# Performance work log

Measured on AMD Instinct MI355X. Metric: run time of the kernel, lower is better.

## Reference

```python
import jax, jax.numpy as jnp
import numpy as np
from math import atanh

B, T, D_IN, H = 16, 1024, 512, 1024
INIT_A = atanh(0.95)


def setup_inputs() -> dict:
    key = jax.random.key(0)
    k1, k2, k3, k4 = jax.random.split(key, 4)
    x = jax.random.normal(k1, (B, T, D_IN), dtype=jnp.float32)
    h0 = jax.random.normal(k2, (B, H), dtype=jnp.float32)
    # raw_a initialized near atanh(0.95) as in the module, with small jitter
    raw_a = INIT_A + 0.01 * jax.random.normal(k3, (H,), dtype=jnp.float32)
    # xavier-uniform for W_x.weight [H, D_IN]
    limit = float(np.sqrt(6.0 / (D_IN + H)))
    W = jax.random.uniform(k4, (H, D_IN), dtype=jnp.float32, minval=-limit, maxval=limit)
    b = jnp.zeros((H,), dtype=jnp.float32)
    return {"x": x, "h0": h0, "raw_a": raw_a, "W": W, "b": b}


def reference(x, h0, raw_a, W, b):
    # h_t = a * h_{t-1} + W x_t + b, computed via cumprod/cumsum parallel-scan trick
    a = jnp.tanh(raw_a)                                   # [H] (rho is None)
    z = jnp.einsum('btd,hd->bth', x, W) + b               # [B,T,H]
    A = jnp.broadcast_to(a, (x.shape[1], a.shape[0]))     # [T,H]
    p = jnp.cumprod(A, axis=0)[None]                      # [1,T,H], p[t] = a^(t+1)
    v = jnp.cumsum(z / jnp.maximum(p, 1e-12), axis=1)     # [B,T,H]
    h = v * p + p * h0[:, None, :]                        # include initial state
    zero_mask = (jnp.abs(a) < 1e-6)[None, None, :]        # degenerate a ~ 0 channels
    h = jnp.where(zero_mask, z, h)
    return h
```

## Files before the change

kernel.cpp:

```cpp
#include <hip/hip_runtime.h>
#include <cstdint>

#define B_DIM 16
#define T_DIM 1024
#define DK    512
#define H_DIM 1024

#define TCH    128
#define NCH    (T_DIM / TCH)
#define NB     128
#define NSTRIP (H_DIM / NB)
#define NKT    16
#define BKQ    4

typedef __bf16 bf16x8 __attribute__((ext_vector_type(8)));
typedef __bf16 bf16x4 __attribute__((ext_vector_type(4)));
typedef float  f32x4  __attribute__((ext_vector_type(4)));

typedef __attribute__((address_space(1))) unsigned int* as1p;
typedef __attribute__((address_space(3))) unsigned int* as3p;

__device__ __forceinline__ void async_cp16(const void* g, void* l) {
  __builtin_amdgcn_global_load_lds((as1p)(uint64_t)g,
                                   (as3p)(uint32_t)(uint64_t)l, 16, 0, 0);
}

__global__ __launch_bounds__(256) void prep(const float* __restrict__ x,
                                            __bf16* __restrict__ xbt,
                                            const float* __restrict__ W,
                                            __bf16* __restrict__ wbT,
                                            const float* __restrict__ raw_a,
                                            float4* __restrict__ meta,
                                            unsigned long long* __restrict__ flags) {
  const int bid = blockIdx.x, tid = threadIdx.x;
  if (bid < 4096) {
    const int g = bid * 256 + tid;
    const int b = g >> 16;
    const int r = g & 65535;
    const int kq = ((r >> 12) << 2) | (tid & 3);
    const int t  = (((r >> 6) & 63) << 4) | ((tid & 63) >> 2);
    const float* src = x + ((size_t)(b * T_DIM + t) * DK + kq * 8);
    f32x4 v0 = ((const f32x4*)src)[0];
    f32x4 v1 = ((const f32x4*)src)[1];
    bf16x8 o;
    o[0] = (__bf16)v0.x; o[1] = (__bf16)v0.y; o[2] = (__bf16)v0.z; o[3] = (__bf16)v0.w;
    o[4] = (__bf16)v1.x; o[5] = (__bf16)v1.y; o[6] = (__bf16)v1.z; o[7] = (__bf16)v1.w;
    *(bf16x8*)(xbt + ((size_t)(b * 64 + kq) * T_DIM + t) * 8) = o;
  } else if (bid < 4608) {
    const int i = (bid - 4096) * 256 + tid;
    const int h  = i >> 7;
    const int k0 = (i & 127) * 4;
    f32x4 v = ((const f32x4*)W)[i];
    bf16x4 o;
    o.x = (__bf16)v.x; o.y = (__bf16)v.y; o.z = (__bf16)v.z; o.w = (__bf16)v.w;
    *(bf16x4*)(wbT + ((size_t)(k0 >> 3) * H_DIM + h) * 8 + (k0 & 7)) = o;
  } else if (bid < 4612) {
    const int h = (bid - 4608) * 256 + tid;
    const float a = tanhf(raw_a[h]);
    const float la2 = log2f(fabsf(a));
    meta[h] = make_float4(a, la2, (a < 0.f) ? 1.f : 0.f, (fabsf(a) < 1e-6f) ? 1.f : 0.f);
  } else {
    flags[(bid - 4612) * 256 + tid] = 0ULL;
  }
}

__global__ __launch_bounds__(256, 3) void fused_rnn(
    const __bf16* __restrict__ xbt,
    const __bf16* __restrict__ wbT,
    const float* __restrict__ bias,
    const float4* __restrict__ meta,
    const float* __restrict__ h0g,
    unsigned long long* __restrict__ flags,
    float* __restrict__ out) {
  __shared__ __align__(16) __bf16 As[3][BKQ][TCH][8];
  __shared__ __align__(16) __bf16 Bs[3][BKQ][NB][8];
  __shared__ float chunkTot[2][NB];
  __shared__ float colCarry[NB];

  const int tid  = threadIdx.x;
  const int wave = tid >> 6;
  const int lane = tid & 63;
  const int q  = lane >> 4;
  const int c  = lane & 15;
  const int rw = wave & 1;
  const int cg = wave >> 1;

  const int bid   = blockIdx.x;
  const int g     = bid & 127;
  const int strip = bid >> 7;
  const int b     = g >> 3;
  const int chunk = g & 7;
  const int t0    = chunk * TCH;
  const int n0    = strip * NB;

  float bias_j[4], la2_j[4], a_j[4], ai_j[4], sgn_j[4], h0_j[4];
  bool zm_j[4];
#pragma unroll
  for (int j = 0; j < 4; ++j) {
    const int col = n0 + cg * 64 + j * 16 + c;
    bias_j[j] = bias[col];
    const float4 mt = meta[col];
    a_j[j]   = mt.x;
    la2_j[j] = mt.y;
    ai_j[j]  = 1.f / mt.x;
    sgn_j[j] = (mt.z != 0.f) ? -1.f : 1.f;
    zm_j[j]  = mt.w != 0.f;
    h0_j[j]  = h0g[(size_t)b * H_DIM + col];
  }

  auto stage = [&](int kt, int buf) {
    const int kq0 = kt * BKQ;
#pragma unroll
    for (int it = 0; it < 2; ++it) {
      const int s = it * 256 + tid;
      const int kq = s >> 7, row = s & 127;
      async_cp16(xbt + ((size_t)(b * 64 + kq0 + kq) * T_DIM + t0 + row) * 8,
                 &As[buf][kq][row][0]);
    }
#pragma unroll
    for (int it = 0; it < 2; ++it) {
      const int s = it * 256 + tid;
      const int kq = s >> 7, col = s & 127;
      async_cp16(wbT + ((size_t)(kq0 + kq) * H_DIM + n0 + col) * 8,
                 &Bs[buf][kq][col][0]);
    }
  };

  f32x4 acc[4][4];
#pragma unroll
  for (int i = 0; i < 4; ++i)
#pragma unroll
    for (int j = 0; j < 4; ++j)
      acc[i][j] = (f32x4){bias_j[j], bias_j[j], bias_j[j], bias_j[j]};

  stage(0, 0); stage(1, 1); stage(2, 2);

  int buf = 0;
  for (int kt = 0; kt < NKT; ++kt) {
    if (kt < NKT - 2)       asm volatile("s_waitcnt vmcnt(8)" ::: "memory");
    else if (kt == NKT - 2) asm volatile("s_waitcnt vmcnt(4)" ::: "memory");
    else                    asm volatile("s_waitcnt vmcnt(0)" ::: "memory");
    __builtin_amdgcn_s_barrier();
    bf16x8 af[4], bfr[4];
#pragma unroll
    for (int i = 0; i < 4; ++i)
      af[i] = *(const bf16x8*)(&As[buf][q][rw * 64 + i * 16 + c][0]);
#pragma unroll
    for (int j = 0; j < 4; ++j)
      bfr[j] = *(const bf16x8*)(&Bs[buf][q][cg * 64 + j * 16 + c][0]);
#pragma unroll
    for (int i = 0; i < 4; ++i)
#pragma unroll
      for (int j = 0; j < 4; ++j)
        acc[i][j] = __builtin_amdgcn_mfma_f32_16x16x32_bf16(af[i], bfr[j], acc[i][j], 0, 0, 0);
    __builtin_amdgcn_sched_barrier(0);
    __builtin_amdgcn_s_barrier();
    if (kt < NKT - 3) stage(kt + 3, buf);
    buf = (buf == 2) ? 0 : buf + 1;
  }

  float base_[4][4];
  float icarry[4] = {0.f, 0.f, 0.f, 0.f};
#pragma unroll
  for (int i = 0; i < 4; ++i) {
    const int tp10 = t0 + rw * 64 + i * 16 + q * 4 + 1;
#pragma unroll
    for (int j = 0; j < 4; ++j) {
      float u = __builtin_amdgcn_exp2f(-la2_j[j] * (float)tp10) * sgn_j[j];
      f32x4 wv;
#pragma unroll
      for (int r = 0; r < 4; ++r) {
        const float uu = fminf(u, 1e12f);
        const float inv = (u < 0.f) ? 1e12f : uu;
        wv[r] = acc[i][j][r] * inv;
        u *= ai_j[j];
      }
      const float pr0 = wv[0];
      const float pr1 = pr0 + wv[1];
      const float pr2 = pr1 + wv[2];
      const float pr3 = pr2 + wv[3];
      const float x1 = __shfl_xor(pr3, 16, 64);
      const float x2 = __shfl_xor(pr3, 32, 64);
      const float x3 = __shfl_xor(pr3, 48, 64);
      float sq = 0.f;
      if (q >= 2) sq += x2 + x3;
      if (q & 1) sq += x1;
      const float base = icarry[j] + sq;
      base_[i][j] = base;
      acc[i][j] = (f32x4){base + pr0, base + pr1, base + pr2, base + pr3};
      icarry[j] += pr3 + x1 + x2 + x3;
    }
  }
  if (q == 0) {
#pragma unroll
    for (int j = 0; j < 4; ++j) chunkTot[rw][cg * 64 + j * 16 + c] = icarry[j];
  }
  __syncthreads();

  if (tid < NB) {
    const int col = tid;
    const size_t fb = ((size_t)b * NSTRIP + strip) * NCH * NB;
    const float tot = chunkTot[0][col] + chunkTot[1][col];
    atomicExch(&flags[fb + (size_t)chunk * NB + col],
               (1ULL << 32) | (unsigned long long)__float_as_uint(tot));
    float s = 0.f;
    for (int p = 0; p < chunk; ++p) {
      unsigned long long v = atomicAdd(&flags[fb + (size_t)p * NB + col], 0ULL);
      while (!(v >> 32)) {
        __builtin_amdgcn_s_sleep(4);
        v = atomicAdd(&flags[fb + (size_t)p * NB + col], 0ULL);
      }
      s += __uint_as_float((unsigned int)v);
    }
    colCarry[col] = s;
  }
  __syncthreads();

  float cc_[4];
#pragma unroll
  for (int j = 0; j < 4; ++j) {
    const int colL = cg * 64 + j * 16 + c;
    float s = colCarry[colL];
    if (rw) s += chunkTot[0][colL];
    cc_[j] = s + h0_j[j];
  }
#pragma unroll
  for (int i = 0; i < 4; ++i) {
    const int tp10 = t0 + rw * 64 + i * 16 + q * 4 + 1;
#pragma unroll
    for (int j = 0; j < 4; ++j) {
      float pv = __builtin_amdgcn_exp2f(la2_j[j] * (float)tp10) * sgn_j[j];
      const int col = n0 + cg * 64 + j * 16 + c;
#pragma unroll
      for (int r = 0; r < 4; ++r) {
        const int tl = t0 + rw * 64 + i * 16 + q * 4 + r;
        const float hv = pv * (acc[i][j][r] + cc_[j]);
        const float wr = acc[i][j][r] - ((r == 0) ? base_[i][j] : acc[i][j][r - 1]);
        out[(size_t)(b * T_DIM + tl) * H_DIM + col] = zm_j[j] ? wr * 1e-12f : hv;
        pv *= a_j[j];
      }
    }
  }
}

extern "C" void kernel_launch(void* const* d_in, const int* in_sizes, int n_in,
                              void* d_out, int out_size, void* d_ws, size_t ws_size,
                              hipStream_t stream) {
  const float* x     = (const float*)d_in[0];
  const float* h0    = (const float*)d_in[1];
  const float* raw_a = (const float*)d_in[2];
  const float* W     = (const float*)d_in[3];
  const float* bias  = (const float*)d_in[4];
  float* out = (float*)d_out;

  char* ws = (char*)d_ws;
  __bf16* xbt = (__bf16*)(ws);
  __bf16* wbT = (__bf16*)(ws + 16777216);
  float4* meta = (float4*)(ws + 16777216 + 1048576);
  unsigned long long* flags =
      (unsigned long long*)(ws + 16777216 + 1048576 + 16384);

  prep<<<5124, 256, 0, stream>>>(x, xbt, W, wbT, raw_a, meta, flags);
  fused_rnn<<<1024, 256, 0, stream>>>(xbt, wbT, bias, meta, h0, flags, out);
}
```

Measured before the change: 124.3 us.

## Fuse x fp32-to-bf16 conversion into GEMM loads, drop separate x prepass

```diff
diff --git a/kernel.cpp b/kernel.cpp
--- a/kernel.cpp
+++ b/kernel.cpp
@@ -11,7 +11,6 @@
 #define NB     128
 #define NSTRIP (H_DIM / NB)
 #define NKT    16
-#define BKQ    4
 
 typedef __bf16 bf16x8 __attribute__((ext_vector_type(8)));
 typedef __bf16 bf16x4 __attribute__((ext_vector_type(4)));
@@ -25,55 +24,40 @@
                                    (as3p)(uint32_t)(uint64_t)l, 16, 0, 0);
 }
 
-__global__ __launch_bounds__(256) void prep(const float* __restrict__ x,
-                                            __bf16* __restrict__ xbt,
-                                            const float* __restrict__ W,
+__global__ __launch_bounds__(256) void prep(const float* __restrict__ W,
                                             __bf16* __restrict__ wbT,
                                             const float* __restrict__ raw_a,
                                             float4* __restrict__ meta,
                                             unsigned long long* __restrict__ flags) {
   const int bid = blockIdx.x, tid = threadIdx.x;
-  if (bid < 4096) {
-    const int g = bid * 256 + tid;
-    const int b = g >> 16;
-    const int r = g & 65535;
-    const int kq = ((r >> 12) << 2) | (tid & 3);
-    const int t  = (((r >> 6) & 63) << 4) | ((tid & 63) >> 2);
-    const float* src = x + ((size_t)(b * T_DIM + t) * DK + kq * 8);
-    f32x4 v0 = ((const f32x4*)src)[0];
-    f32x4 v1 = ((const f32x4*)src)[1];
-    bf16x8 o;
-    o[0] = (__bf16)v0.x; o[1] = (__bf16)v0.y; o[2] = (__bf16)v0.z; o[3] = (__bf16)v0.w;
-    o[4] = (__bf16)v1.x; o[5] = (__bf16)v1.y; o[6] = (__bf16)v1.z; o[7] = (__bf16)v1.w;
-    *(bf16x8*)(xbt + ((size_t)(b * 64 + kq) * T_DIM + t) * 8) = o;
-  } else if (bid < 4608) {
-    const int i = (bid - 4096) * 256 + tid;
+  if (bid < 512) {
+    const int i = bid * 256 + tid;
     const int h  = i >> 7;
     const int k0 = (i & 127) * 4;
     f32x4 v = ((const f32x4*)W)[i];
     bf16x4 o;
     o.x = (__bf16)v.x; o.y = (__bf16)v.y; o.z = (__bf16)v.z; o.w = (__bf16)v.w;
     *(bf16x4*)(wbT + ((size_t)(k0 >> 3) * H_DIM + h) * 8 + (k0 & 7)) = o;
-  } else if (bid < 4612) {
-    const int h = (bid - 4608) * 256 + tid;
+  } else if (bid < 516) {
+    const int h = (bid - 512) * 256 + tid;
     const float a = tanhf(raw_a[h]);
     const float la2 = log2f(fabsf(a));
     meta[h] = make_float4(a, la2, (a < 0.f) ? 1.f : 0.f, (fabsf(a) < 1e-6f) ? 1.f : 0.f);
   } else {
-    flags[(bid - 4612) * 256 + tid] = 0ULL;
+    flags[(bid - 516) * 256 + tid] = 0ULL;
   }
 }
 
 __global__ __launch_bounds__(256, 3) void fused_rnn(
-    const __bf16* __restrict__ xbt,
+    const float* __restrict__ xf,
     const __bf16* __restrict__ wbT,
     const float* __restrict__ bias,
     const float4* __restrict__ meta,
     const float* __restrict__ h0g,
     unsigned long long* __restrict__ flags,
     float* __restrict__ out) {
-  __shared__ __align__(16) __bf16 As[3][BKQ][TCH][8];
-  __shared__ __align__(16) __bf16 Bs[3][BKQ][NB][8];
+  __shared__ __align__(16) float  Asf[2][8][TCH][4];
+  __shared__ __align__(16) __bf16 Bs[2][4][NB][8];
   __shared__ float chunkTot[2][NB];
   __shared__ float colCarry[NB];
 
@@ -93,12 +77,72 @@
   const int t0    = chunk * TCH;
   const int n0    = strip * NB;
 
-  float bias_j[4], la2_j[4], a_j[4], ai_j[4], sgn_j[4], h0_j[4];
+  float bias_j[4];
+#pragma unroll
+  for (int j = 0; j < 4; ++j) bias_j[j] = bias[n0 + cg * 64 + j * 16 + c];
+
+  const float* const xB = xf + (size_t)(b * T_DIM + t0) * DK;
+
+  auto stage = [&](int kt, int buf) {
+#pragma unroll
+    for (int it = 0; it < 4; ++it) {
+      const int s = it * 256 + tid;
+      const int kq4 = s >> 7, row = s & 127;
+      async_cp16(xB + (size_t)row * DK + kt * 32 + kq4 * 4,
+                 &Asf[buf][kq4][row][0]);
+    }
+#pragma unroll
+    for (int it = 0; it < 2; ++it) {
+      const int s = it * 256 + tid;
+      const int kq = s >> 7, col = s & 127;
+      async_cp16(wbT + ((size_t)(kt * 4 + kq) * H_DIM + n0 + col) * 8,
+                 &Bs[buf][kq][col][0]);
+    }
+  };
+
+  f32x4 acc[4][4];
+#pragma unroll
+  for (int i = 0; i < 4; ++i)
+#pragma unroll
+    for (int j = 0; j < 4; ++j)
+      acc[i][j] = (f32x4){bias_j[j], bias_j[j], bias_j[j], bias_j[j]};
+
+  stage(0, 0); stage(1, 1);
+
+  for (int kt = 0; kt < NKT; ++kt) {
+    const int buf = kt & 1;
+    if (kt < NKT - 1) asm volatile("s_waitcnt vmcnt(6)" ::: "memory");
+    else              asm volatile("s_waitcnt vmcnt(0)" ::: "memory");
+    __builtin_amdgcn_s_barrier();
+    bf16x8 af[4], bfr[4];
+#pragma unroll
+    for (int i = 0; i < 4; ++i) {
+      const int row = rw * 64 + i * 16 + c;
+      const f32x4 a0 = *(const f32x4*)(&Asf[buf][2 * q][row][0]);
+      const f32x4 a1 = *(const f32x4*)(&Asf[buf][2 * q + 1][row][0]);
+      bf16x8 t;
+      t[0] = (__bf16)a0.x; t[1] = (__bf16)a0.y; t[2] = (__bf16)a0.z; t[3] = (__bf16)a0.w;
+      t[4] = (__bf16)a1.x; t[5] = (__bf16)a1.y; t[6] = (__bf16)a1.z; t[7] = (__bf16)a1.w;
+      af[i] = t;
+    }
+#pragma unroll
+    for (int j = 0; j < 4; ++j)
+      bfr[j] = *(const bf16x8*)(&Bs[buf][q][cg * 64 + j * 16 + c][0]);
+#pragma unroll
+    for (int i = 0; i < 4; ++i)
+#pragma unroll
+      for (int j = 0; j < 4; ++j)
+        acc[i][j] = __builtin_amdgcn_mfma_f32_16x16x32_bf16(af[i], bfr[j], acc[i][j], 0, 0, 0);
+    __builtin_amdgcn_sched_barrier(0);
+    __builtin_amdgcn_s_barrier();
+    if (kt < NKT - 2) stage(kt + 2, buf);
+  }
+
+  float la2_j[4], a_j[4], ai_j[4], sgn_j[4], h0_j[4];
   bool zm_j[4];
 #pragma unroll
   for (int j = 0; j < 4; ++j) {
     const int col = n0 + cg * 64 + j * 16 + c;
-    bias_j[j] = bias[col];
     const float4 mt = meta[col];
     a_j[j]   = mt.x;
     la2_j[j] = mt.y;
@@ -106,57 +150,6 @@
     sgn_j[j] = (mt.z != 0.f) ? -1.f : 1.f;
     zm_j[j]  = mt.w != 0.f;
     h0_j[j]  = h0g[(size_t)b * H_DIM + col];
-  }
-
-  auto stage = [&](int kt, int buf) {
-    const int kq0 = kt * BKQ;
-#pragma unroll
-    for (int it = 0; it < 2; ++it) {
-      const int s = it * 256 + tid;
-      const int kq = s >> 7, row = s & 127;
-      async_cp16(xbt + ((size_t)(b * 64 + kq0 + kq) * T_DIM + t0 + row) * 8,
-                 &As[buf][kq][row][0]);
-    }
-#pragma unroll
-    for (int it = 0; it < 2; ++it) {
-      const int s = it * 256 + tid;
-      const int kq = s >> 7, col = s & 127;
-      async_cp16(wbT + ((size_t)(kq0 + kq) * H_DIM + n0 + col) * 8,
-                 &Bs[buf][kq][col][0]);
-    }
-  };
-
-  f32x4 acc[4][4];
-#pragma unroll
-  for (int i = 0; i < 4; ++i)
-#pragma unroll
-    for (int j = 0; j < 4; ++j)
-      acc[i][j] = (f32x4){bias_j[j], bias_j[j], bias_j[j], bias_j[j]};
-
-  stage(0, 0); stage(1, 1); stage(2, 2);
-
-  int buf = 0;
-  for (int kt = 0; kt < NKT; ++kt) {
-    if (kt < NKT - 2)       asm volatile("s_waitcnt vmcnt(8)" ::: "memory");
-    else if (kt == NKT - 2) asm volatile("s_waitcnt vmcnt(4)" ::: "memory");
-    else                    asm volatile("s_waitcnt vmcnt(0)" ::: "memory");
-    __builtin_amdgcn_s_barrier();
-    bf16x8 af[4], bfr[4];
-#pragma unroll
-    for (int i = 0; i < 4; ++i)
-      af[i] = *(const bf16x8*)(&As[buf][q][rw * 64 + i * 16 + c][0]);
-#pragma unroll
-    for (int j = 0; j < 4; ++j)
-      bfr[j] = *(const bf16x8*)(&Bs[buf][q][cg * 64 + j * 16 + c][0]);
-#pragma unroll
-    for (int i = 0; i < 4; ++i)
-#pragma unroll
-      for (int j = 0; j < 4; ++j)
-        acc[i][j] = __builtin_amdgcn_mfma_f32_16x16x32_bf16(af[i], bfr[j], acc[i][j], 0, 0, 0);
-    __builtin_amdgcn_sched_barrier(0);
-    __builtin_amdgcn_s_barrier();
-    if (kt < NKT - 3) stage(kt + 3, buf);
-    buf = (buf == 2) ? 0 : buf + 1;
   }
 
   float base_[4][4];
@@ -254,12 +247,11 @@
   float* out = (float*)d_out;
 
   char* ws = (char*)d_ws;
-  __bf16* xbt = (__bf16*)(ws);
-  __bf16* wbT = (__bf16*)(ws + 16777216);
-  float4* meta = (float4*)(ws + 16777216 + 1048576);
+  __bf16* wbT = (__bf16*)(ws);
+  float4* meta = (float4*)(ws + 1048576);
   unsigned long long* flags =
-      (unsigned long long*)(ws + 16777216 + 1048576 + 16384);
-
-  prep<<<5124, 256, 0, stream>>>(x, xbt, W, wbT, raw_a, meta, flags);
-  fused_rnn<<<1024, 256, 0, stream>>>(xbt, wbT, bias, meta, h0, flags, out);
-}
+      (unsigned long long*)(ws + 1048576 + 16384);
+
+  prep<<<1028, 256, 0, stream>>>(W, wbT, raw_a, meta, flags);
+  fused_rnn<<<1024, 256, 0, stream>>>(x, wbT, bias, meta, h0, flags, out);
+}
```

Result: slower. 145.9 us (+17.3%).

## Load A fragments directly to registers and deepen B LDS pipeline

Applied to the files above, without the earlier changes.

```diff
diff --git a/kernel.cpp b/kernel.cpp
--- a/kernel.cpp
+++ b/kernel.cpp
@@ -11,7 +11,6 @@
 #define NB     128
 #define NSTRIP (H_DIM / NB)
 #define NKT    16
-#define BKQ    4
 
 typedef __bf16 bf16x8 __attribute__((ext_vector_type(8)));
 typedef __bf16 bf16x4 __attribute__((ext_vector_type(4)));
@@ -64,7 +63,7 @@
   }
 }
 
-__global__ __launch_bounds__(256, 3) void fused_rnn(
+__global__ __launch_bounds__(256, 4) void fused_rnn(
     const __bf16* __restrict__ xbt,
     const __bf16* __restrict__ wbT,
     const float* __restrict__ bias,
@@ -72,10 +71,8 @@
     const float* __restrict__ h0g,
     unsigned long long* __restrict__ flags,
     float* __restrict__ out) {
-  __shared__ __align__(16) __bf16 As[3][BKQ][TCH][8];
-  __shared__ __align__(16) __bf16 Bs[3][BKQ][NB][8];
-  __shared__ float chunkTot[2][NB];
-  __shared__ float colCarry[NB];
+  __shared__ __align__(16) __bf16 Bs[4][4][NB][8];
+  float* const scr = (float*)&Bs[0][0][0][0];
 
   const int tid  = threadIdx.x;
   const int wave = tid >> 6;
@@ -93,12 +90,75 @@
   const int t0    = chunk * TCH;
   const int n0    = strip * NB;
 
-  float bias_j[4], la2_j[4], a_j[4], ai_j[4], sgn_j[4], h0_j[4];
+  float bias_j[4];
+#pragma unroll
+  for (int j = 0; j < 4; ++j) bias_j[j] = bias[n0 + cg * 64 + j * 16 + c];
+
+  const __bf16* const xA =
+      xbt + ((size_t)(b * 64 + q) * T_DIM + t0 + rw * 64 + c) * 8;
+
+  auto stageB = [&](int kt) {
+    const int buf = kt & 3;
+#pragma unroll
+    for (int it = 0; it < 2; ++it) {
+      const int s = it * 256 + tid;
+      const int kq = s >> 7, col = s & 127;
+      async_cp16(wbT + ((size_t)(kt * 4 + kq) * H_DIM + n0 + col) * 8,
+                 &Bs[buf][kq][col][0]);
+    }
+  };
+
+  f32x4 acc[4][4];
+#pragma unroll
+  for (int i = 0; i < 4; ++i)
+#pragma unroll
+    for (int j = 0; j < 4; ++j)
+      acc[i][j] = (f32x4){bias_j[j], bias_j[j], bias_j[j], bias_j[j]};
+
+  bf16x8 afA[4], afB[4];
+
+  stageB(0); stageB(1); stageB(2);
+#pragma unroll
+  for (int i = 0; i < 4; ++i) afA[i] = *(const bf16x8*)(xA + i * 128);
+
+  auto body = [&](int kt, bf16x8 (&cur)[4], bf16x8 (&nxt)[4]) {
+    const int buf = kt & 3;
+    if (kt <= NKT - 3)      asm volatile("s_waitcnt vmcnt(8)" ::: "memory");
+    else if (kt == NKT - 2) asm volatile("s_waitcnt vmcnt(6)" ::: "memory");
+    else                    asm volatile("s_waitcnt vmcnt(4)" ::: "memory");
+    __builtin_amdgcn_s_barrier();
+    __builtin_amdgcn_sched_barrier(0);
+    if (kt + 3 < NKT) stageB(kt + 3);
+    if (kt + 1 < NKT) {
+      const __bf16* p = xA + (size_t)(kt + 1) * 32768;
+#pragma unroll
+      for (int i = 0; i < 4; ++i) nxt[i] = *(const bf16x8*)(p + i * 128);
+    }
+    bf16x8 b0 = *(const bf16x8*)(&Bs[buf][q][cg * 64 + 0 * 16 + c][0]);
+    bf16x8 b1 = *(const bf16x8*)(&Bs[buf][q][cg * 64 + 1 * 16 + c][0]);
+#pragma unroll
+    for (int i = 0; i < 4; ++i) {
+      acc[i][0] = __builtin_amdgcn_mfma_f32_16x16x32_bf16(cur[i], b0, acc[i][0], 0, 0, 0);
+      acc[i][1] = __builtin_amdgcn_mfma_f32_16x16x32_bf16(cur[i], b1, acc[i][1], 0, 0, 0);
+    }
+    bf16x8 b2 = *(const bf16x8*)(&Bs[buf][q][cg * 64 + 2 * 16 + c][0]);
+    bf16x8 b3 = *(const bf16x8*)(&Bs[buf][q][cg * 64 + 3 * 16 + c][0]);
+#pragma unroll
+    for (int i = 0; i < 4; ++i) {
+      acc[i][2] = __builtin_amdgcn_mfma_f32_16x16x32_bf16(cur[i], b2, acc[i][2], 0, 0, 0);
+      acc[i][3] = __builtin_amdgcn_mfma_f32_16x16x32_bf16(cur[i], b3, acc[i][3], 0, 0, 0);
+    }
+  };
+  for (int kt2 = 0; kt2 < NKT; kt2 += 2) {
+    body(kt2,     afA, afB);
+    body(kt2 + 1, afB, afA);
+  }
+
+  float la2_j[4], a_j[4], ai_j[4], sgn_j[4], h0_j[4];
   bool zm_j[4];
 #pragma unroll
   for (int j = 0; j < 4; ++j) {
     const int col = n0 + cg * 64 + j * 16 + c;
-    bias_j[j] = bias[col];
     const float4 mt = meta[col];
     a_j[j]   = mt.x;
     la2_j[j] = mt.y;
@@ -106,57 +166,6 @@
     sgn_j[j] = (mt.z != 0.f) ? -1.f : 1.f;
     zm_j[j]  = mt.w != 0.f;
     h0_j[j]  = h0g[(size_t)b * H_DIM + col];
-  }
-
-  auto stage = [&](int kt, int buf) {
-    const int kq0 = kt * BKQ;
-#pragma unroll
-    for (int it = 0; it < 2; ++it) {
-      const int s = it * 256 + tid;
-      const int kq = s >> 7, row = s & 127;
-      async_cp16(xbt + ((size_t)(b * 64 + kq0 + kq) * T_DIM + t0 + row) * 8,
-                 &As[buf][kq][row][0]);
-    }
-#pragma unroll
-    for (int it = 0; it < 2; ++it) {
-      const int s = it * 256 + tid;
-      const int kq = s >> 7, col = s & 127;
-      async_cp16(wbT + ((size_t)(kq0 + kq) * H_DIM + n0 + col) * 8,
-                 &Bs[buf][kq][col][0]);
-    }
-  };
-
-  f32x4 acc[4][4];
-#pragma unroll
-  for (int i = 0; i < 4; ++i)
-#pragma unroll
-    for (int j = 0; j < 4; ++j)
-      acc[i][j] = (f32x4){bias_j[j], bias_j[j], bias_j[j], bias_j[j]};
-
-  stage(0, 0); stage(1, 1); stage(2, 2);
-
-  int buf = 0;
-  for (int kt = 0; kt < NKT; ++kt) {
-    if (kt < NKT - 2)       asm volatile("s_waitcnt vmcnt(8)" ::: "memory");
-    else if (kt == NKT - 2) asm volatile("s_waitcnt vmcnt(4)" ::: "memory");
-    else                    asm volatile("s_waitcnt vmcnt(0)" ::: "memory");
-    __builtin_amdgcn_s_barrier();
-    bf16x8 af[4], bfr[4];
-#pragma unroll
-    for (int i = 0; i < 4; ++i)
-      af[i] = *(const bf16x8*)(&As[buf][q][rw * 64 + i * 16 + c][0]);
-#pragma unroll
-    for (int j = 0; j < 4; ++j)
-      bfr[j] = *(const bf16x8*)(&Bs[buf][q][cg * 64 + j * 16 + c][0]);
-#pragma unroll
-    for (int i = 0; i < 4; ++i)
-#pragma unroll
-      for (int j = 0; j < 4; ++j)
-        acc[i][j] = __builtin_amdgcn_mfma_f32_16x16x32_bf16(af[i], bfr[j], acc[i][j], 0, 0, 0);
-    __builtin_amdgcn_sched_barrier(0);
-    __builtin_amdgcn_s_barrier();
-    if (kt < NKT - 3) stage(kt + 3, buf);
-    buf = (buf == 2) ? 0 : buf + 1;
   }
 
   float base_[4][4];
@@ -193,26 +202,26 @@
   }
   if (q == 0) {
 #pragma unroll
-    for (int j = 0; j < 4; ++j) chunkTot[rw][cg * 64 + j * 16 + c] = icarry[j];
+    for (int j = 0; j < 4; ++j) scr[rw * NB + cg * 64 + j * 16 + c] = icarry[j];
   }
   __syncthreads();
 
   if (tid < NB) {
     const int col = tid;
     const size_t fb = ((size_t)b * NSTRIP + strip) * NCH * NB;
-    const float tot = chunkTot[0][col] + chunkTot[1][col];
+    const float tot = scr[col] + scr[NB + col];
     atomicExch(&flags[fb + (size_t)chunk * NB + col],
                (1ULL << 32) | (unsigned long long)__float_as_uint(tot));
     float s = 0.f;
     for (int p = 0; p < chunk; ++p) {
       unsigned long long v = atomicAdd(&flags[fb + (size_t)p * NB + col], 0ULL);
       while (!(v >> 32)) {
-        __builtin_amdgcn_s_sleep(4);
+        __builtin_amdgcn_s_sleep(8);
         v = atomicAdd(&flags[fb + (size_t)p * NB + col], 0ULL);
       }
       s += __uint_as_float((unsigned int)v);
     }
-    colCarry[col] = s;
+    scr[2 * NB + col] = s;
   }
   __syncthreads();
 
@@ -220,8 +229,8 @@
 #pragma unroll
   for (int j = 0; j < 4; ++j) {
     const int colL = cg * 64 + j * 16 + c;
-    float s = colCarry[colL];
-    if (rw) s += chunkTot[0][colL];
+    float s = scr[2 * NB + colL];
+    if (rw) s += scr[colL];
     cc_[j] = s + h0_j[j];
   }
 #pragma unroll
```

Measured after the change: 137.2 us. 1.1x slower.
